# Kernel optimization log

Measured on AMD Instinct MI355X. Metric: run time of the kernel, lower is better.

The kernel has to match this reference:

```python
import jax, jax.numpy as jnp
import numpy as np

B, CITY, H, E, IN = 512, 100, 256, 256, 2
D2 = 2 * H  # num_directions * hidden_size
PEN = 1e6   # already_played_penalty


def _cell(x, h, c, Wih, Whh, b):
    # PyTorch LSTM cell, gate order i,f,g,o
    g = x @ Wih.T + h @ Whh.T + b
    i, f, gg, o = jnp.split(g, 4, axis=-1)
    c = jax.nn.sigmoid(f) * c + jax.nn.sigmoid(i) * jnp.tanh(gg)
    h = jax.nn.sigmoid(o) * jnp.tanh(c)
    return h, c


def _run_lstm(xs, Wih, Whh, b, reverse):
    # xs: [B, T, E] -> outputs [B, T, H], final (h, c)
    Bsz, hdim = xs.shape[0], Whh.shape[1]
    init = (jnp.zeros((Bsz, hdim), xs.dtype), jnp.zeros((Bsz, hdim), xs.dtype))
    def step(carry, x):
        h, c = _cell(x, carry[0], carry[1], Wih, Whh, b)
        return (h, c), h
    (h, c), hs = jax.lax.scan(step, init, jnp.swapaxes(xs, 0, 1), reverse=reverse)
    return jnp.swapaxes(hs, 0, 1), h, c


def setup_inputs() -> dict:
    key = jax.random.key(0)
    ks = iter(jax.random.split(key, 32))
    nrm = lambda shape: 0.1 * jax.random.normal(next(ks), shape, dtype=jnp.float32)
    return {
        "inputs": jax.random.normal(next(ks), (B, CITY, IN), dtype=jnp.float32),
        "test_roads": jax.random.randint(next(ks), (B, CITY), 0, CITY, dtype=jnp.int32),
        "W_embed": nrm((E, IN)),
        "enc_Wih_f": nrm((4 * H, E)), "enc_Whh_f": nrm((4 * H, H)), "enc_b_f": nrm((4 * H,)),
        "enc_Wih_b": nrm((4 * H, E)), "enc_Whh_b": nrm((4 * H, H)), "enc_b_b": nrm((4 * H,)),
        "dec_Wih_f": nrm((4 * H, D2)), "dec_Whh_f": nrm((4 * H, H)), "dec_b_f": nrm((4 * H,)),
        "dec_Wih_b": nrm((4 * H, D2)), "dec_Whh_b": nrm((4 * H, H)), "dec_b_b": nrm((4 * H,)),
        "W_ref": nrm((D2, D2)), "W_q": nrm((D2, D2)), "v": nrm((D2,)),
        "W_ref2": nrm((D2, D2)), "W_q2": nrm((D2, D2)), "v2": nrm((D2,)),
    }


def _forward(inputs, test_roads, W_embed,
             enc_Wih_f, enc_Whh_f, enc_b_f, enc_Wih_b, enc_Whh_b, enc_b_b,
             dec_Wih_f, dec_Whh_f, dec_b_f, dec_Wih_b, dec_Whh_b, dec_b_b,
             W_ref, W_q, v, W_ref2, W_q2, v2):
    Bsz, city, _ = inputs.shape
    emb = inputs @ W_embed.T                                  # [B, city, E]
    enc_f, hf0, cf0 = _run_lstm(emb, enc_Wih_f, enc_Whh_f, enc_b_f, False)
    enc_b, hb0, cb0 = _run_lstm(emb, enc_Wih_b, enc_Whh_b, enc_b_b, True)
    Enc = jnp.concatenate([enc_f, enc_b], axis=-1)            # [B, city, D2]
    # dropout p=0 -> Enc is loop-invariant; hoist the two ref projections
    ref1 = Enc @ W_ref.T                                      # [B, city, D2]
    ref2 = Enc @ W_ref2.T                                     # [B, city, D2]

    def step(carry, tgt):
        x, hf, cf, hb, cb, played, loss = carry
        hf, cf = _cell(x, hf, cf, dec_Wih_f, dec_Whh_f, dec_b_f)
        hb, cb = _cell(x, hb, cb, dec_Wih_b, dec_Whh_b, dec_b_b)
        dec_out = jnp.concatenate([hf, hb], axis=-1)          # [B, D2]
        ow = jnp.tanh(ref1 + (dec_out @ W_q.T)[:, None, :]) @ v - PEN * played   # [B, city]
        aw = jax.nn.softmax(jnp.tanh(ref2 + (x @ W_q2.T)[:, None, :]) @ v2, axis=1)
        sel = jnp.argmax(ow, axis=1)                          # [B]
        x_new = jnp.einsum('bj,bjk->bk', aw, Enc)             # [B, D2]
        played = played + jax.nn.one_hot(sel, city, dtype=played.dtype)
        ce = jax.nn.logsumexp(ow, axis=1) - jnp.take_along_axis(ow, tgt[:, None], axis=1)[:, 0]
        return (x_new, hf, cf, hb, cb, played, loss + ce), None

    x0 = jnp.zeros((Bsz, Enc.shape[-1]), inputs.dtype)
    played0 = jnp.zeros((Bsz, city), inputs.dtype)
    loss0 = jnp.zeros((Bsz,), inputs.dtype)
    carry, _ = jax.lax.scan(step, (x0, hf0, cf0, hb0, cb0, played0, loss0),
                            test_roads.T.astype(jnp.int32))
    return carry[-1]                                          # path_loss [B]


def reference(inputs, test_roads, W_embed,
              enc_Wih_f, enc_Whh_f, enc_b_f, enc_Wih_b, enc_Whh_b, enc_b_b,
              dec_Wih_f, dec_Whh_f, dec_b_f, dec_Wih_b, dec_Whh_b, dec_b_b,
              W_ref, W_q, v, W_ref2, W_q2, v2):
    return _forward(inputs, test_roads, W_embed,
                    enc_Wih_f, enc_Whh_f, enc_b_f, enc_Wih_b, enc_Whh_b, enc_b_b,
                    dec_Wih_f, dec_Whh_f, dec_b_f, dec_Wih_b, dec_Whh_b, dec_b_b,
                    W_ref, W_q, v, W_ref2, W_q2, v2)
```

## Files before the change

kernel.cpp:

```cpp
#include <hip/hip_runtime.h>
#include <hip/hip_fp16.h>
#include <math.h>

namespace {
constexpr int Bn  = 512;
constexpr int Tn  = 100;
constexpr int Hn  = 256;
constexpr int En  = 256;
constexpr int D2n = 512;
constexpr int G4n = 1024;
constexpr float PENf = 1e6f;
constexpr size_t BIGN = (size_t)Bn * Tn * D2n;
constexpr int FLAG_STRIDE = 32;
constexpr int DBLK = 896;
constexpr size_t BAR_UINTS = (256 + DBLK) * FLAG_STRIDE + 64;
}

using short8  = __attribute__((ext_vector_type(8))) short;
using us8     = __attribute__((ext_vector_type(8))) unsigned short;
using floatx4 = __attribute__((ext_vector_type(4))) float;

template<typename T> __device__ __forceinline__ float cvt_to_f(T x);
template<> __device__ __forceinline__ float cvt_to_f<float>(float x) { return x; }
template<> __device__ __forceinline__ float cvt_to_f<__half>(__half x) {
  return __half2float(x);
}
template<typename T> __device__ __forceinline__ T cvt_from_f(float x);
template<> __device__ __forceinline__ float cvt_from_f<float>(float x) { return x; }
template<> __device__ __forceinline__ __half cvt_from_f<__half>(float x) {
  return __float2half(x);
}
__device__ __forceinline__ float h2f_bits(unsigned short b) {
  __half_raw r; r.x = b; return __half2float(__half(r));
}
__device__ __forceinline__ float fast_exp(float x) {
  return __builtin_amdgcn_exp2f(x * 1.44269504088896340736f);
}
__device__ __forceinline__ float sigmoidf(float x) {
  return __builtin_amdgcn_rcpf(1.0f + fast_exp(-x));
}
__device__ __forceinline__ float fast_tanhf(float x) {
  return 1.0f - 2.0f * __builtin_amdgcn_rcpf(fast_exp(2.0f * x) + 1.0f);
}

__device__ __forceinline__ float loadf_dev(const float* p) {
  return __uint_as_float(__hip_atomic_load((const unsigned*)p, __ATOMIC_RELAXED,
                                           __HIP_MEMORY_SCOPE_AGENT));
}
__device__ __forceinline__ void storef_dev(float* p, float v) {
  __hip_atomic_store((unsigned*)p, __float_as_uint(v), __ATOMIC_RELAXED,
                     __HIP_MEMORY_SCOPE_AGENT);
}
__device__ __forceinline__ float4 load4_dev(const float* p) {
  const unsigned long long a = __hip_atomic_load((const unsigned long long*)p,
      __ATOMIC_RELAXED, __HIP_MEMORY_SCOPE_AGENT);
  const unsigned long long b = __hip_atomic_load((const unsigned long long*)p + 1,
      __ATOMIC_RELAXED, __HIP_MEMORY_SCOPE_AGENT);
  float4 r;
  r.x = __uint_as_float((unsigned)a);  r.y = __uint_as_float((unsigned)(a >> 32));
  r.z = __uint_as_float((unsigned)b);  r.w = __uint_as_float((unsigned)(b >> 32));
  return r;
}
__device__ __forceinline__ void store2_dev(float* p, const float2 v) {
  const unsigned long long a = (unsigned long long)__float_as_uint(v.x) |
                               ((unsigned long long)__float_as_uint(v.y) << 32);
  __hip_atomic_store((unsigned long long*)p, a, __ATOMIC_RELAXED,
                     __HIP_MEMORY_SCOPE_AGENT);
}
template<typename CT> __device__ __forceinline__ CT load_dev(const CT* p);
template<> __device__ __forceinline__ float load_dev<float>(const float* p) {
  return loadf_dev(p);
}
template<> __device__ __forceinline__ __half load_dev<__half>(const __half* p) {
  unsigned short u = __hip_atomic_load((const unsigned short*)p, __ATOMIC_RELAXED,
                                       __HIP_MEMORY_SCOPE_AGENT);
  __half_raw r; r.x = u; return (__half)r;
}
template<typename CT> __device__ __forceinline__ void store_dev(CT* p, CT v);
template<> __device__ __forceinline__ void store_dev<float>(float* p, float v) {
  storef_dev(p, v);
}
template<> __device__ __forceinline__ void store_dev<__half>(__half* p, __half v) {
  __half_raw r = *reinterpret_cast<__half_raw*>(&v);
  __hip_atomic_store((unsigned short*)p, r.x, __ATOMIC_RELAXED,
                     __HIP_MEMORY_SCOPE_AGENT);
}

__device__ __forceinline__ void split2(float x, short& h, short& l) {
  const unsigned u  = __float_as_uint(x);
  const unsigned hu = u & 0xffff0000u;
  h = (short)(hu >> 16);
  const float r = x - __uint_as_float(hu);
  l = (short)((__float_as_uint(r) + 0x8000u) >> 16);
}
__device__ __forceinline__ void store4split(const float4 v, short* hp, short* lp) {
  short h0, h1, h2, h3, l0, l1, l2, l3;
  split2(v.x, h0, l0); split2(v.y, h1, l1);
  split2(v.z, h2, l2); split2(v.w, h3, l3);
  *(short4*)hp = make_short4(h0, h1, h2, h3);
  *(short4*)lp = make_short4(l0, l1, l2, l3);
}

__device__ __forceinline__ void grid_sync256(unsigned* flags, unsigned* release,
                                             unsigned no) {
  __builtin_amdgcn_s_waitcnt(0);
  __syncthreads();
  if (blockIdx.x == 0) {
    const int tid = threadIdx.x;
    if (tid > 0) {
      while (__hip_atomic_load(&flags[tid * FLAG_STRIDE], __ATOMIC_RELAXED,
                               __HIP_MEMORY_SCOPE_AGENT) < no)
        __builtin_amdgcn_s_sleep(1);
    }
    __syncthreads();
    if (tid == 0)
      __hip_atomic_store(release, no, __ATOMIC_RELAXED, __HIP_MEMORY_SCOPE_AGENT);
  } else {
    if (threadIdx.x == 0) {
      __hip_atomic_store(&flags[blockIdx.x * FLAG_STRIDE], no, __ATOMIC_RELAXED,
                         __HIP_MEMORY_SCOPE_AGENT);
      while (__hip_atomic_load(release, __ATOMIC_RELAXED,
                               __HIP_MEMORY_SCOPE_AGENT) < no)
        __builtin_amdgcn_s_sleep(2);
    }
    __syncthreads();
  }
}

__device__ __forceinline__ void grid_syncD(unsigned* flags, unsigned* release,
                                           unsigned no) {
  __builtin_amdgcn_s_waitcnt(0);
  __syncthreads();
  if (blockIdx.x == 0) {
    for (int i = threadIdx.x; i < DBLK; i += 256) {
      if (i > 0) {
        while (__hip_atomic_load(&flags[i * FLAG_STRIDE], __ATOMIC_RELAXED,
                                 __HIP_MEMORY_SCOPE_AGENT) < no)
          __builtin_amdgcn_s_sleep(1);
      }
    }
    __syncthreads();
    if (threadIdx.x == 0)
      __hip_atomic_store(release, no, __ATOMIC_RELAXED, __HIP_MEMORY_SCOPE_AGENT);
  } else {
    if (threadIdx.x == 0) {
      __hip_atomic_store(&flags[blockIdx.x * FLAG_STRIDE], no, __ATOMIC_RELAXED,
                         __HIP_MEMORY_SCOPE_AGENT);
      while (__hip_atomic_load(release, __ATOMIC_RELAXED,
                               __HIP_MEMORY_SCOPE_AGENT) < no)
        __builtin_amdgcn_s_sleep(2);
    }
    __syncthreads();
  }
}

template<typename CT, bool ACC, int NT, bool CSC>
__device__ __forceinline__ void gemm64v2(short* smem,
    const float* A, int lda, int m0,
    const float* B, int ldb, int n0, int K,
    CT* Cbase, size_t crstride, int tid) {
  constexpr int BPL  = NT * 128;
  constexpr int BSZ  = NT * 512;
  constexpr int BUFS = 4096 + 2 * BSZ;
  const int lane = tid & 63, wave = tid >> 6, qm = lane & 15, quad = lane >> 4;
  const int ra = tid >> 3, c4 = tid & 7, j0 = (c4 & 1) * 4, gq = c4 >> 1;
  const int a0 = gq * 512 + ra * 8 + j0;
  const int a1 = gq * 512 + (ra + 32) * 8 + j0;
  const int b0 = gq * BPL + ra * 8 + j0;
  const int b1 = gq * BPL + (ra + 32) * 8 + j0;
  const int CN = K >> 5;

  floatx4 acc[NT];
#pragma unroll
  for (int nt = 0; nt < NT; ++nt) acc[nt] = (floatx4){0.f, 0.f, 0.f, 0.f};

  float4 Aa0, Aa1, Ba0, Ba1, Ab0, Ab1, Bb0, Bb1;
  auto ld = [&](int c, float4& x0, float4& x1, float4& y0, float4& y1) {
    const int k0 = c * 32 + c4 * 4;
    x0 = load4_dev(A + (size_t)(m0 + ra) * lda + k0);
    x1 = load4_dev(A + (size_t)(m0 + ra + 32) * lda + k0);
    y0 = *(const float4*)(B + (size_t)(n0 + ra) * ldb + k0);
    if (NT == 4)
      y1 = *(const float4*)(B + (size_t)(n0 + ra + 32) * ldb + k0);
  };
  auto st = [&](short* bp, const float4& x0, const float4& x1,
                const float4& y0, const float4& y1) {
    store4split(x0, bp + a0, bp + 2048 + a0);
    store4split(x1, bp + a1, bp + 2048 + a1);
    store4split(y0, bp + 4096 + b0, bp + 4096 + BSZ + b0);
    if (NT == 4) store4split(y1, bp + 4096 + b1, bp + 4096 + BSZ + b1);
  };
  auto mm = [&](const short* bp) {
    const int abase = quad * 512 + (wave * 16 + qm) * 8;
    const short8 ah = *(const short8*)&bp[abase];
    const short8 al = *(const short8*)&bp[2048 + abase];
#pragma unroll
    for (int nt = 0; nt < NT; ++nt) {
      const int bb = quad * BPL + (nt * 16 + qm) * 8;
      const short8 bh = *(const short8*)&bp[4096 + bb];
      const short8 bl = *(const short8*)&bp[4096 + BSZ + bb];
      acc[nt] = __builtin_amdgcn_mfma_f32_16x16x32_bf16(ah, bh, acc[nt], 0, 0, 0);
      acc[nt] = __builtin_amdgcn_mfma_f32_16x16x32_bf16(ah, bl, acc[nt], 0, 0, 0);
      acc[nt] = __builtin_amdgcn_mfma_f32_16x16x32_bf16(al, bh, acc[nt], 0, 0, 0);
    }
  };

  ld(0, Aa0, Aa1, Ba0, Ba1);
  if (CN > 1) ld(1, Ab0, Ab1, Bb0, Bb1);
  st(smem, Aa0, Aa1, Ba0, Ba1);
  __syncthreads();
  for (int c = 0; c < CN; c += 2) {
    if (c + 2 < CN) ld(c + 2, Aa0, Aa1, Ba0, Ba1);
    mm(smem);
    if (c + 1 < CN) st(smem + BUFS, Ab0, Ab1, Bb0, Bb1);
    __syncthreads();
    if (c + 1 < CN) {
      if (c + 3 < CN) ld(c + 3, Ab0, Ab1, Bb0, Bb1);
      mm(smem + BUFS);
      if (c + 2 < CN) st(smem, Aa0, Aa1, Ba0, Ba1);
      __syncthreads();
    }
  }

#pragma unroll
  for (int nt = 0; nt < NT; ++nt)
#pragma unroll
    for (int r2 = 0; r2 < 4; ++r2) {
      const int m = wave * 16 + quad * 4 + r2, n = nt * 16 + qm;
      CT* cp = Cbase + (size_t)m * crstride + n;
      float o = acc[nt][r2];
      if (CSC) {
        if (ACC) o += cvt_to_f<CT>(load_dev<CT>(cp));
        store_dev<CT>(cp, cvt_from_f<CT>(o));
      } else {
        if (ACC) o += cvt_to_f<CT>(*cp);
        *cp = cvt_from_f<CT>(o);
      }
    }
}

__device__ __forceinline__ void gates_gemm_v2(floatx4 acc[4], short* smem,
    const float* A1, int lda1, const float* B1, int ldb1, int K1,
    const float* A2, int lda2, const float* B2, int ldb2, int K2,
    int m0, int hoff, int tid) {
  const int lane = tid & 63, wave = tid >> 6, qm = lane & 15, quad = lane >> 4;
  const int ra = tid >> 3, c4 = tid & 7, j0 = (c4 & 1) * 4, gq = c4 >> 1;
  const int a0 = gq * 512 + ra * 8 + j0;
  const int a1 = gq * 512 + (ra + 32) * 8 + j0;
  const int g0 = (ra >> 4) * Hn + hoff + (ra & 15);
  const int g1 = ((ra + 32) >> 4) * Hn + hoff + ((ra + 32) & 15);
  const int C1 = K1 >> 5;
  const int C2 = A2 ? (K2 >> 5) : 0;
  const int CN = C1 + C2;

  float4 Aa0, Aa1, Ba0, Ba1, Ab0, Ab1, Bb0, Bb1;
  auto ld = [&](int c, float4& x0, float4& x1, float4& y0, float4& y1) {
    const float* A; const float* B; int lda, ldb, k0;
    if (c < C1) { A = A1; B = B1; lda = lda1; ldb = ldb1; k0 = c * 32; }
    else        { A = A2; B = B2; lda = lda2; ldb = ldb2; k0 = (c - C1) * 32; }
    k0 += c4 * 4;
    x0 = load4_dev(A + (size_t)(m0 + ra) * lda + k0);
    x1 = load4_dev(A + (size_t)(m0 + ra + 32) * lda + k0);
    y0 = *(const float4*)(B + (size_t)g0 * ldb + k0);
    y1 = *(const float4*)(B + (size_t)g1 * ldb + k0);
  };
  auto st2 = [&](short* bp, const float4& x0, const float4& x1,
                 const float4& y0, const float4& y1) {
    store4split(x0, bp + a0, bp + 2048 + a0);
    store4split(x1, bp + a1, bp + 2048 + a1);
    store4split(y0, bp + 4096 + a0, bp + 6144 + a0);
    store4split(y1, bp + 4096 + a1, bp + 6144 + a1);
  };
  auto mm = [&](const short* bp) {
    const int abase = quad * 512 + (wave * 16 + qm) * 8;
    const short8 ah = *(const short8*)&bp[abase];
    const short8 al = *(const short8*)&bp[2048 + abase];
#pragma unroll
    for (int gg = 0; gg < 4; ++gg) {
      const int bb = quad * 512 + (gg * 16 + qm) * 8;
      const short8 bh = *(const short8*)&bp[4096 + bb];
      const short8 bl = *(const short8*)&bp[6144 + bb];
      acc[gg] = __builtin_amdgcn_mfma_f32_16x16x32_bf16(ah, bh, acc[gg], 0, 0, 0);
      acc[gg] = __builtin_amdgcn_mfma_f32_16x16x32_bf16(ah, bl, acc[gg], 0, 0, 0);
      acc[gg] = __builtin_amdgcn_mfma_f32_16x16x32_bf16(al, bh, acc[gg], 0, 0, 0);
    }
  };

  if (CN <= 0) return;
  ld(0, Aa0, Aa1, Ba0, Ba1);
  if (CN > 1) ld(1, Ab0, Ab1, Bb0, Bb1);
  st2(smem, Aa0, Aa1, Ba0, Ba1);
  __syncthreads();
  for (int c = 0; c < CN; c += 2) {
    if (c + 2 < CN) ld(c + 2, Aa0, Aa1, Ba0, Ba1);
    mm(smem);
    if (c + 1 < CN) st2(smem + 8192, Ab0, Ab1, Bb0, Bb1);
    __syncthreads();
    if (c + 1 < CN) {
      if (c + 3 < CN) ld(c + 3, Ab0, Ab1, Bb0, Bb1);
      mm(smem + 8192);
      if (c + 2 < CN) st2(smem, Aa0, Aa1, Ba0, Ba1);
      __syncthreads();
    }
  }
}

__global__ void weff_kernel(const float* Wih_f, const float* Wih_b,
                            const float* W_embed, float* weff_f, float* weff_b) {
  const int gidx = blockIdx.x * 256 + threadIdx.x;
  if (gidx >= G4n) return;
  float f0 = 0.f, f1 = 0.f, b0 = 0.f, b1 = 0.f;
  for (int e = 0; e < En; ++e) {
    const float w0 = W_embed[e * 2 + 0];
    const float w1 = W_embed[e * 2 + 1];
    const float wf = Wih_f[gidx * En + e];
    const float wb = Wih_b[gidx * En + e];
    f0 = fmaf(wf, w0, f0); f1 = fmaf(wf, w1, f1);
    b0 = fmaf(wb, w0, b0); b1 = fmaf(wb, w1, b1);
  }
  weff_f[gidx * 2 + 0] = f0; weff_f[gidx * 2 + 1] = f1;
  weff_b[gidx * 2 + 0] = b0; weff_b[gidx * 2 + 1] = b1;
}

template<typename ET, typename RT1, typename RT2>
struct EncP {
  const float* inputs;
  const float* Whh_f; const float* Whh_b;
  const float* b_f; const float* b_b;
  const float* weff_f; const float* weff_b;
  const float* W_ref; const float* W_ref2;
  float* hbuf;
  float* c_dec;
  float* dec_out0;
  ET* Enc; RT1* ref1; RT2* ref2;
  unsigned* flags; unsigned* release;
};

template<typename ET, typename RT1, typename RT2>
__global__ __launch_bounds__(256, 1) void enc_coop(EncP<ET, RT1, RT2> P) {
  __shared__ __align__(16) short smem[16384];
  const int bid = blockIdx.x, tid = threadIdx.x;
  const int dir = bid >> 7, btile = (bid >> 4) & 7, hs = bid & 15;
  const int r_ref = (bid >> 7) & 1, r_dir = (bid >> 6) & 1;
  const int r_bt = (bid >> 3) & 7, r_ns = bid & 7;
  const int lane = tid & 63, wave = tid >> 6, qm = lane & 15, quad = lane >> 4;
  const int hcol = hs * 16 + qm;
  const float* Whh  = dir ? P.Whh_b : P.Whh_f;
  const float* bias = dir ? P.b_b : P.b_f;
  const float* weff = dir ? P.weff_b : P.weff_f;
  float c_reg[4] = {0.f, 0.f, 0.f, 0.f};
  float h_reg[4] = {0.f, 0.f, 0.f, 0.f};
  unsigned sync_no = 0;

  auto ref_job = [&](const float* hpar, int pos) {
    const float* hsrc = hpar + (size_t)r_dir * (Bn * Hn);
    if (r_ref == 0)
      gemm64v2<RT1, true, 4, true>(smem, hsrc, Hn, r_bt * 64,
                             P.W_ref + r_dir * Hn, D2n, r_ns * 64, Hn,
                             P.ref1 + (size_t)(r_bt * 64) * Tn * D2n + (size_t)pos * D2n + r_ns * 64,
                             (size_t)Tn * D2n, tid);
    else
      gemm64v2<RT2, true, 4, true>(smem, hsrc, Hn, r_bt * 64,
                             P.W_ref2 + r_dir * Hn, D2n, r_ns * 64, Hn,
                             P.ref2 + (size_t)(r_bt * 64) * Tn * D2n + (size_t)pos * D2n + r_ns * 64,
                             (size_t)Tn * D2n, tid);
  };

  for (int t = 0; t < Tn; ++t) {
    const float* hprev = P.hbuf + (size_t)((t - 1) & 1) * (2 * Bn * Hn);
    if (t > 0) ref_job(hprev, r_dir ? (Tn - t) : (t - 1));
    floatx4 acc[4];
#pragma unroll
    for (int gg = 0; gg < 4; ++gg) acc[gg] = (floatx4){0.f, 0.f, 0.f, 0.f};
    if (t > 0)
      gates_gemm_v2(acc, smem, hprev + (size_t)dir * (Bn * Hn), Hn, Whh, Hn, Hn,
                    nullptr, 0, nullptr, 0, 0, btile * 64, hs * 16, tid);
    const int tcur = dir ? (Tn - 1 - t) : t;
    float xa[4], xb2[4];
#pragma unroll
    for (int r2 = 0; r2 < 4; ++r2) {
      const int m = btile * 64 + wave * 16 + quad * 4 + r2;
      xa[r2]  = P.inputs[(size_t)m * (Tn * 2) + tcur * 2 + 0];
      xb2[r2] = P.inputs[(size_t)m * (Tn * 2) + tcur * 2 + 1];
    }
    float gv[4][4];
#pragma unroll
    for (int gg = 0; gg < 4; ++gg) {
      const int grow = gg * Hn + hcol;
      const float bn = bias[grow];
      const float w20 = weff[grow * 2], w21 = weff[grow * 2 + 1];
#pragma unroll
      for (int r2 = 0; r2 < 4; ++r2) {
        float o = acc[gg][r2] + bn;
        o = fmaf(xa[r2], w20, fmaf(xb2[r2], w21, o));
        gv[gg][r2] = o;
      }
    }
    float* hdst = P.hbuf + (size_t)(t & 1) * (2 * Bn * Hn) + (size_t)dir * (Bn * Hn);
    const int tt = dir ? (Tn - 1 - t) : t;
#pragma unroll
    for (int r2 = 0; r2 < 4; ++r2) {
      const float cn = sigmoidf(gv[1][r2]) * c_reg[r2] +
                       sigmoidf(gv[0][r2]) * fast_tanhf(gv[2][r2]);
      c_reg[r2] = cn;
      const float hn = sigmoidf(gv[3][r2]) * fast_tanhf(cn);
      h_reg[r2] = hn;
      const int m = btile * 64 + wave * 16 + quad * 4 + r2;
      storef_dev(&hdst[(size_t)m * Hn + hcol], hn);
      store_dev<ET>(&P.Enc[(size_t)m * Tn * D2n + (size_t)tt * D2n + dir * Hn + hcol],
                    cvt_from_f<ET>(hn));
    }
    grid_sync256(P.flags, P.release, ++sync_no);
  }
  ref_job(P.hbuf + (size_t)1 * (2 * Bn * Hn), r_dir ? 0 : (Tn - 1));
#pragma unroll
  for (int r2 = 0; r2 < 4; ++r2) {
    const int m = btile * 64 + wave * 16 + quad * 4 + r2;
    P.dec_out0[(size_t)m * D2n + dir * Hn + hcol] = h_reg[r2];
    P.c_dec[((size_t)dir * Bn + m) * Hn + hcol] = c_reg[r2];
  }
}

template<typename ET, typename RT1, typename RT2>
struct DecP {
  const int* test_roads;
  const float* Wih_f; const float* Whh_f; const float* b_f;
  const float* Wih_b; const float* Whh_b; const float* b_b;
  const float* W_q; const float* W_q2; const float* v; const float* v2;
  const ET* Enc; const RT1* ref1; const RT2* ref2;
  float* dec_out;
  float* xb;
  float* qb; float* q2b;
  const float* c_init;
  float* loss;
  unsigned* flags; unsigned* release;
};

template<typename ET, typename RT1, typename RT2>
__global__ __launch_bounds__(256, 4) void dec_coop(DecP<ET, RT1, RT2> P) {
  __shared__ __align__(16) short smem[16384];
  __shared__ float sl[104], playedl[104];
  __shared__ float wmax[4], wsum[4], dpart[4];
  __shared__ int   widx[4];
  __shared__ float lossl;
  const int bid = blockIdx.x, tid = threadIdx.x;
  const int lane = tid & 63, wave = tid >> 6, qm = lane & 15, quad = lane >> 4;
  const int role = (bid < 256) ? 0 : (bid < 384 ? 1 : 2);

  const int dir = (bid >> 7) & 1, btile = (bid >> 4) & 7, hs = bid & 15;
  const int hcol = hs * 16 + qm;
  const float* Wih  = dir ? P.Wih_b : P.Wih_f;
  const float* Whh  = dir ? P.Whh_b : P.Whh_f;
  const float* bias = dir ? P.b_b : P.b_f;
  float c_reg[4] = {0.f, 0.f, 0.f, 0.f};
  if (role == 0) {
#pragma unroll
    for (int r2 = 0; r2 < 4; ++r2) {
      const int m = btile * 64 + wave * 16 + quad * 4 + r2;
      c_reg[r2] = P.c_init[((size_t)dir * Bn + m) * Hn + hcol];
    }
  }
  const int gidx = bid - 256, pbt = gidx >> 4, pn = gidx & 15;
  const int b = bid - 384;
  if (role == 2) {
    if (tid < Tn) playedl[tid] = 0.f;
    if (tid == 0) lossl = 0.f;
  }
  unsigned sync_no = 0;
  __syncthreads();

  auto s1_fused = [&](int u) {
    const int e = lane * 8;
    const float4 qa = load4_dev(P.qb + (size_t)b * D2n + e);
    const float4 qc = load4_dev(P.qb + (size_t)b * D2n + e + 4);
    const float4 va = *(const float4*)(P.v + e);
    const float4 vb2 = *(const float4*)(P.v + e + 4);
    const float q[8]  = {qa.x, qa.y, qa.z, qa.w, qc.x, qc.y, qc.z, qc.w};
    const float vv[8] = {va.x, va.y, va.z, va.w, vb2.x, vb2.y, vb2.z, vb2.w};
    const unsigned short* pr = (const unsigned short*)P.ref1 +
        (size_t)b * Tn * D2n + (size_t)(wave * 25) * D2n + e;
    us8 r0 = *(const us8*)pr;
    us8 r1 = *(const us8*)(pr + (size_t)D2n);
    us8 r2v = *(const us8*)(pr + (size_t)2 * D2n);
    float bmax = -INFINITY, sume = 0.f; int bidx = 0;
    for (int jj = 0; jj < 25; ++jj) {
      const int row = wave * 25 + jj;
      float a = 0.f;
#pragma unroll
      for (int k = 0; k < 8; ++k)
        a = fmaf(vv[k], fast_tanhf(h2f_bits(r0[k]) + q[k]), a);
      r0 = r1; r1 = r2v;
      if (jj + 3 < 25) r2v = *(const us8*)(pr + (size_t)(jj + 3) * D2n);
#pragma unroll
      for (int off = 32; off > 0; off >>= 1) a += __shfl_xor(a, off, 64);
      if (lane == 0) sl[row] = a;
      const float ow = a - PENf * playedl[row];
      if (ow > bmax) { bmax = ow; bidx = row; }
      sume += fast_exp(ow - 16.f);
    }
    if (lane == 0) { wmax[wave] = bmax; widx[wave] = bidx; wsum[wave] = sume; }
    __syncthreads();
    if (tid == 0) {
      float bv = wmax[0], es = wsum[0]; int bi = widx[0];
#pragma unroll
      for (int w = 1; w < 4; ++w) {
        es += wsum[w];
        if (wmax[w] > bv) { bv = wmax[w]; bi = widx[w]; }
      }
      const int tgt = P.test_roads[b * Tn + u];
      const float owt = sl[tgt] - PENf * playedl[tgt];
      lossl += (16.f + __logf(es)) - owt;
      playedl[bi] += 1.f;
    }
  };

  auto s2x_fused = [&]() {
    const int e = lane * 8;
    const float4 qa = load4_dev(P.q2b + (size_t)b * D2n + e);
    const float4 qc = load4_dev(P.q2b + (size_t)b * D2n + e + 4);
    const float4 va = *(const float4*)(P.v2 + e);
    const float4 vb2 = *(const float4*)(P.v2 + e + 4);
    const float q[8]  = {qa.x, qa.y, qa.z, qa.w, qc.x, qc.y, qc.z, qc.w};
    const float vv[8] = {va.x, va.y, va.z, va.w, vb2.x, vb2.y, vb2.z, vb2.w};
    const unsigned short* pr = (const unsigned short*)P.ref2 +
        (size_t)b * Tn * D2n + (size_t)(wave * 25) * D2n + e;
    const unsigned short* pe = (const unsigned short*)P.Enc +
        (size_t)b * Tn * D2n + (size_t)(wave * 25) * D2n + e;
    us8 r0 = *(const us8*)pr;
    us8 r1 = *(const us8*)(pr + (size_t)D2n);
    us8 r2v = *(const us8*)(pr + (size_t)2 * D2n);
    us8 e0 = *(const us8*)pe;
    us8 e1 = *(const us8*)(pe + (size_t)D2n);
    us8 e2v = *(const us8*)(pe + (size_t)2 * D2n);
    float xacc[8];
#pragma unroll
    for (int k = 0; k < 8; ++k) xacc[k] = 0.f;
    float den = 0.f;
    for (int jj = 0; jj < 25; ++jj) {
      float a = 0.f;
#pragma unroll
      for (int k = 0; k < 8; ++k)
        a = fmaf(vv[k], fast_tanhf(h2f_bits(r0[k]) + q[k]), a);
      r0 = r1; r1 = r2v;
      if (jj + 3 < 25) r2v = *(const us8*)(pr + (size_t)(jj + 3) * D2n);
#pragma unroll
      for (int off = 32; off > 0; off >>= 1) a += __shfl_xor(a, off, 64);
      const float w = fast_exp(a - 16.f);
      den += w;
#pragma unroll
      for (int k = 0; k < 8; ++k)
        xacc[k] = fmaf(w, h2f_bits(e0[k]), xacc[k]);
      e0 = e1; e1 = e2v;
      if (jj + 3 < 25) e2v = *(const us8*)(pe + (size_t)(jj + 3) * D2n);
    }
    float* xpart = (float*)smem;
#pragma unroll
    for (int k = 0; k < 8; ++k) xpart[wave * 512 + e + k] = xacc[k];
    if (lane == 0) dpart[wave] = den;
    __syncthreads();
    {
      const float dsum = dpart[0] + dpart[1] + dpart[2] + dpart[3];
      const float inv = __builtin_amdgcn_rcpf(dsum);
      const int c = tid * 2;
      float2 s;
      s.x = (xpart[c] + xpart[512 + c] + xpart[1024 + c] + xpart[1536 + c]) * inv;
      s.y = (xpart[c + 1] + xpart[512 + c + 1] + xpart[1024 + c + 1] +
             xpart[1536 + c + 1]) * inv;
      store2_dev(&P.xb[(size_t)b * D2n + c], s);
    }
  };

  for (int t = 0; t < Tn; ++t) {
    const float* dcur = P.dec_out + (size_t)(t & 1) * (Bn * D2n);
    float* dnext = P.dec_out + (size_t)((t + 1) & 1) * (Bn * D2n);
    if (role == 0) {
      floatx4 acc[4];
#pragma unroll
      for (int gg = 0; gg < 4; ++gg) acc[gg] = (floatx4){0.f, 0.f, 0.f, 0.f};
      gates_gemm_v2(acc, smem, P.xb, D2n, Wih, D2n, D2n,
                    dcur + dir * Hn, D2n, Whh, Hn, Hn, btile * 64, hs * 16, tid);
#pragma unroll
      for (int gg = 0; gg < 4; ++gg) {
        const float bn = bias[gg * Hn + hcol];
#pragma unroll
        for (int r2 = 0; r2 < 4; ++r2) acc[gg][r2] += bn;
      }
#pragma unroll
      for (int r2 = 0; r2 < 4; ++r2) {
        const float cn = sigmoidf(acc[1][r2]) * c_reg[r2] +
                         sigmoidf(acc[0][r2]) * fast_tanhf(acc[2][r2]);
        c_reg[r2] = cn;
        const float hn = sigmoidf(acc[3][r2]) * fast_tanhf(cn);
        const int m = btile * 64 + wave * 16 + quad * 4 + r2;
        storef_dev(&dnext[(size_t)m * D2n + dir * Hn + hcol], hn);
      }
    } else if (role == 1) {
      gemm64v2<float, false, 2, true>(smem, P.xb, D2n, pbt * 64,
                                      P.W_q2, D2n, pn * 32, D2n,
                                      P.q2b + (size_t)(pbt * 64) * D2n + pn * 32,
                                      D2n, tid);
    } else if (t > 0) {
      s1_fused(t - 1);
    }
    grid_syncD(P.flags, P.release, ++sync_no);
    if (role == 1) {
      gemm64v2<float, false, 2, true>(smem, dnext, D2n, pbt * 64,
                                      P.W_q, D2n, pn * 32, D2n,
                                      P.qb + (size_t)(pbt * 64) * D2n + pn * 32,
                                      D2n, tid);
    } else if (role == 2) {
      s2x_fused();
    }
    grid_syncD(P.flags, P.release, ++sync_no);
  }
  if (role == 2) {
    s1_fused(Tn - 1);
    if (tid == 0) P.loss[b] = lossl;
  }
}

static void run_all(void* const* d_in, void* d_out, char* ws, hipStream_t stream) {
  using ET = __half; using RT1 = __half; using RT2 = __half;
  const float* inputs     = (const float*)d_in[0];
  const int*   test_roads = (const int*)d_in[1];
  const float* W_embed    = (const float*)d_in[2];
  const float* enc_Wih_f  = (const float*)d_in[3];
  const float* enc_Whh_f  = (const float*)d_in[4];
  const float* enc_b_f    = (const float*)d_in[5];
  const float* enc_Wih_b  = (const float*)d_in[6];
  const float* enc_Whh_b  = (const float*)d_in[7];
  const float* enc_b_b    = (const float*)d_in[8];
  const float* dec_Wih_f  = (const float*)d_in[9];
  const float* dec_Whh_f  = (const float*)d_in[10];
  const float* dec_b_f    = (const float*)d_in[11];
  const float* dec_Wih_b  = (const float*)d_in[12];
  const float* dec_Whh_b  = (const float*)d_in[13];
  const float* dec_b_b    = (const float*)d_in[14];
  const float* W_ref      = (const float*)d_in[15];
  const float* W_q        = (const float*)d_in[16];
  const float* v          = (const float*)d_in[17];
  const float* W_ref2     = (const float*)d_in[18];
  const float* W_q2       = (const float*)d_in[19];
  const float* v2         = (const float*)d_in[20];

  char* p0 = ws;
  ET*  Enc  = (ET*)p0;  p0 += BIGN * sizeof(ET);
  RT1* ref1 = (RT1*)p0; p0 += BIGN * sizeof(RT1);
  RT2* ref2 = (RT2*)p0; p0 += BIGN * sizeof(RT2);
  unsigned* flagsE = (unsigned*)p0;
  unsigned* relE   = flagsE + 256 * FLAG_STRIDE;
  unsigned* flagsD = relE + 32;
  unsigned* relD   = flagsD + DBLK * FLAG_STRIDE;
  float* xb      = (float*)(p0 + BAR_UINTS * 4);
  float* dec_out = xb + Bn * D2n;
  float* hbuf    = dec_out + 2 * Bn * D2n;
  float* c_dec   = hbuf + 4 * Bn * Hn;
  float* qb      = c_dec + 2 * Bn * Hn;
  float* q2b     = qb + Bn * D2n;
  float* weff_f  = q2b + Bn * D2n;
  float* weff_b  = weff_f + G4n * 2;

  hipMemsetAsync(ref1, 0, BIGN * (sizeof(RT1) + sizeof(RT2)), stream);
  hipMemsetAsync(flagsE, 0, BAR_UINTS * 4 + (size_t)Bn * D2n * 4, stream);

  weff_kernel<<<G4n / 256, 256, 0, stream>>>(enc_Wih_f, enc_Wih_b, W_embed,
                                             weff_f, weff_b);

  EncP<ET, RT1, RT2> ep = { inputs, enc_Whh_f, enc_Whh_b, enc_b_f, enc_b_b,
                            weff_f, weff_b, W_ref, W_ref2,
                            hbuf, c_dec, dec_out, Enc, ref1, ref2,
                            flagsE, relE };
  enc_coop<ET, RT1, RT2><<<256, 256, 0, stream>>>(ep);

  DecP<ET, RT1, RT2> dp = { test_roads,
                            dec_Wih_f, dec_Whh_f, dec_b_f,
                            dec_Wih_b, dec_Whh_b, dec_b_b,
                            W_q, W_q2, v, v2,
                            Enc, ref1, ref2,
                            dec_out, xb, qb, q2b, c_dec,
                            (float*)d_out, flagsD, relD };
  dec_coop<ET, RT1, RT2><<<DBLK, 256, 0, stream>>>(dp);
}

extern "C" void kernel_launch(void* const* d_in, const int* in_sizes, int n_in,
                              void* d_out, int out_size, void* d_ws, size_t ws_size,
                              hipStream_t stream) {
  (void)in_sizes; (void)n_in; (void)out_size; (void)ws_size;
  run_all(d_in, d_out, (char*)d_ws, stream);
}
```

Before: 7.862 ms.

## Split encoder grid into separate recurrence and ref-projection block groups

The encoder cooperative kernel grows from 256 to 512 blocks. The first 256 blocks run only the LSTM recurrence, and the other 256 compute the W_ref/W_ref2 projections of the previous step's hidden state. Before, each block did both jobs one after the other inside the critical recurrence step; now the projection work runs alongside the recurrence. The cost is a grid barrier over twice as many blocks and a need for two blocks per CU (launch bounds raised to 2), which may pressure registers and LDS.

```diff
diff --git a/kernel.cpp b/kernel.cpp
--- a/kernel.cpp
+++ b/kernel.cpp
@@ -12,8 +12,9 @@
 constexpr float PENf = 1e6f;
 constexpr size_t BIGN = (size_t)Bn * Tn * D2n;
 constexpr int FLAG_STRIDE = 32;
+constexpr int EBLK = 512;
 constexpr int DBLK = 896;
-constexpr size_t BAR_UINTS = (256 + DBLK) * FLAG_STRIDE + 64;
+constexpr size_t BAR_UINTS = (EBLK + DBLK) * FLAG_STRIDE + 64;
 }
 
 using short8  = __attribute__((ext_vector_type(8))) short;
@@ -101,38 +102,13 @@
   *(short4*)lp = make_short4(l0, l1, l2, l3);
 }
 
-__device__ __forceinline__ void grid_sync256(unsigned* flags, unsigned* release,
-                                             unsigned no) {
-  __builtin_amdgcn_s_waitcnt(0);
-  __syncthreads();
-  if (blockIdx.x == 0) {
-    const int tid = threadIdx.x;
-    if (tid > 0) {
-      while (__hip_atomic_load(&flags[tid * FLAG_STRIDE], __ATOMIC_RELAXED,
-                               __HIP_MEMORY_SCOPE_AGENT) < no)
-        __builtin_amdgcn_s_sleep(1);
-    }
-    __syncthreads();
-    if (tid == 0)
-      __hip_atomic_store(release, no, __ATOMIC_RELAXED, __HIP_MEMORY_SCOPE_AGENT);
-  } else {
-    if (threadIdx.x == 0) {
-      __hip_atomic_store(&flags[blockIdx.x * FLAG_STRIDE], no, __ATOMIC_RELAXED,
-                         __HIP_MEMORY_SCOPE_AGENT);
-      while (__hip_atomic_load(release, __ATOMIC_RELAXED,
-                               __HIP_MEMORY_SCOPE_AGENT) < no)
-        __builtin_amdgcn_s_sleep(2);
-    }
-    __syncthreads();
-  }
-}
-
-__device__ __forceinline__ void grid_syncD(unsigned* flags, unsigned* release,
+template<int NB>
+__device__ __forceinline__ void grid_syncN(unsigned* flags, unsigned* release,
                                            unsigned no) {
   __builtin_amdgcn_s_waitcnt(0);
   __syncthreads();
   if (blockIdx.x == 0) {
-    for (int i = threadIdx.x; i < DBLK; i += 256) {
+    for (int i = threadIdx.x; i < NB; i += 256) {
       if (i > 0) {
         while (__hip_atomic_load(&flags[i * FLAG_STRIDE], __ATOMIC_RELAXED,
                                  __HIP_MEMORY_SCOPE_AGENT) < no)
@@ -337,12 +313,14 @@
 };
 
 template<typename ET, typename RT1, typename RT2>
-__global__ __launch_bounds__(256, 1) void enc_coop(EncP<ET, RT1, RT2> P) {
+__global__ __launch_bounds__(256, 2) void enc_coop(EncP<ET, RT1, RT2> P) {
   __shared__ __align__(16) short smem[16384];
   const int bid = blockIdx.x, tid = threadIdx.x;
-  const int dir = bid >> 7, btile = (bid >> 4) & 7, hs = bid & 15;
-  const int r_ref = (bid >> 7) & 1, r_dir = (bid >> 6) & 1;
-  const int r_bt = (bid >> 3) & 7, r_ns = bid & 7;
+  const bool gr = bid < 256;
+  const int dir = (bid >> 7) & 1, btile = (bid >> 4) & 7, hs = bid & 15;
+  const int rbid = bid - 256;
+  const int r_ref = (rbid >> 7) & 1, r_dir = (rbid >> 6) & 1;
+  const int r_bt = (rbid >> 3) & 7, r_ns = rbid & 7;
   const int lane = tid & 63, wave = tid >> 6, qm = lane & 15, quad = lane >> 4;
   const int hcol = hs * 16 + qm;
   const float* Whh  = dir ? P.Whh_b : P.Whh_f;
@@ -368,56 +346,62 @@
 
   for (int t = 0; t < Tn; ++t) {
     const float* hprev = P.hbuf + (size_t)((t - 1) & 1) * (2 * Bn * Hn);
-    if (t > 0) ref_job(hprev, r_dir ? (Tn - t) : (t - 1));
-    floatx4 acc[4];
-#pragma unroll
-    for (int gg = 0; gg < 4; ++gg) acc[gg] = (floatx4){0.f, 0.f, 0.f, 0.f};
-    if (t > 0)
-      gates_gemm_v2(acc, smem, hprev + (size_t)dir * (Bn * Hn), Hn, Whh, Hn, Hn,
-                    nullptr, 0, nullptr, 0, 0, btile * 64, hs * 16, tid);
-    const int tcur = dir ? (Tn - 1 - t) : t;
-    float xa[4], xb2[4];
+    if (gr) {
+      floatx4 acc[4];
+#pragma unroll
+      for (int gg = 0; gg < 4; ++gg) acc[gg] = (floatx4){0.f, 0.f, 0.f, 0.f};
+      if (t > 0)
+        gates_gemm_v2(acc, smem, hprev + (size_t)dir * (Bn * Hn), Hn, Whh, Hn, Hn,
+                      nullptr, 0, nullptr, 0, 0, btile * 64, hs * 16, tid);
+      const int tcur = dir ? (Tn - 1 - t) : t;
+      float xa[4], xb2[4];
+#pragma unroll
+      for (int r2 = 0; r2 < 4; ++r2) {
+        const int m = btile * 64 + wave * 16 + quad * 4 + r2;
+        xa[r2]  = P.inputs[(size_t)m * (Tn * 2) + tcur * 2 + 0];
+        xb2[r2] = P.inputs[(size_t)m * (Tn * 2) + tcur * 2 + 1];
+      }
+      float gv[4][4];
+#pragma unroll
+      for (int gg = 0; gg < 4; ++gg) {
+        const int grow = gg * Hn + hcol;
+        const float bn = bias[grow];
+        const float w20 = weff[grow * 2], w21 = weff[grow * 2 + 1];
+#pragma unroll
+        for (int r2 = 0; r2 < 4; ++r2) {
+          float o = acc[gg][r2] + bn;
+          o = fmaf(xa[r2], w20, fmaf(xb2[r2], w21, o));
+          gv[gg][r2] = o;
+        }
+      }
+      float* hdst = P.hbuf + (size_t)(t & 1) * (2 * Bn * Hn) + (size_t)dir * (Bn * Hn);
+      const int tt = dir ? (Tn - 1 - t) : t;
+#pragma unroll
+      for (int r2 = 0; r2 < 4; ++r2) {
+        const float cn = sigmoidf(gv[1][r2]) * c_reg[r2] +
+                         sigmoidf(gv[0][r2]) * fast_tanhf(gv[2][r2]);
+        c_reg[r2] = cn;
+        const float hn = sigmoidf(gv[3][r2]) * fast_tanhf(cn);
+        h_reg[r2] = hn;
+        const int m = btile * 64 + wave * 16 + quad * 4 + r2;
+        storef_dev(&hdst[(size_t)m * Hn + hcol], hn);
+        store_dev<ET>(&P.Enc[(size_t)m * Tn * D2n + (size_t)tt * D2n + dir * Hn + hcol],
+                      cvt_from_f<ET>(hn));
+      }
+    } else if (t > 0) {
+      ref_job(hprev, r_dir ? (Tn - t) : (t - 1));
+    }
+    grid_syncN<EBLK>(P.flags, P.release, ++sync_no);
+  }
+  if (!gr) {
+    ref_job(P.hbuf + (size_t)1 * (2 * Bn * Hn), r_dir ? 0 : (Tn - 1));
+  } else {
 #pragma unroll
     for (int r2 = 0; r2 < 4; ++r2) {
       const int m = btile * 64 + wave * 16 + quad * 4 + r2;
-      xa[r2]  = P.inputs[(size_t)m * (Tn * 2) + tcur * 2 + 0];
-      xb2[r2] = P.inputs[(size_t)m * (Tn * 2) + tcur * 2 + 1];
-    }
-    float gv[4][4];
-#pragma unroll
-    for (int gg = 0; gg < 4; ++gg) {
-      const int grow = gg * Hn + hcol;
-      const float bn = bias[grow];
-      const float w20 = weff[grow * 2], w21 = weff[grow * 2 + 1];
-#pragma unroll
-      for (int r2 = 0; r2 < 4; ++r2) {
-        float o = acc[gg][r2] + bn;
-        o = fmaf(xa[r2], w20, fmaf(xb2[r2], w21, o));
-        gv[gg][r2] = o;
-      }
-    }
-    float* hdst = P.hbuf + (size_t)(t & 1) * (2 * Bn * Hn) + (size_t)dir * (Bn * Hn);
-    const int tt = dir ? (Tn - 1 - t) : t;
-#pragma unroll
-    for (int r2 = 0; r2 < 4; ++r2) {
-      const float cn = sigmoidf(gv[1][r2]) * c_reg[r2] +
-                       sigmoidf(gv[0][r2]) * fast_tanhf(gv[2][r2]);
-      c_reg[r2] = cn;
-      const float hn = sigmoidf(gv[3][r2]) * fast_tanhf(cn);
-      h_reg[r2] = hn;
-      const int m = btile * 64 + wave * 16 + quad * 4 + r2;
-      storef_dev(&hdst[(size_t)m * Hn + hcol], hn);
-      store_dev<ET>(&P.Enc[(size_t)m * Tn * D2n + (size_t)tt * D2n + dir * Hn + hcol],
-                    cvt_from_f<ET>(hn));
-    }
-    grid_sync256(P.flags, P.release, ++sync_no);
-  }
-  ref_job(P.hbuf + (size_t)1 * (2 * Bn * Hn), r_dir ? 0 : (Tn - 1));
-#pragma unroll
-  for (int r2 = 0; r2 < 4; ++r2) {
-    const int m = btile * 64 + wave * 16 + quad * 4 + r2;
-    P.dec_out0[(size_t)m * D2n + dir * Hn + hcol] = h_reg[r2];
-    P.c_dec[((size_t)dir * Bn + m) * Hn + hcol] = c_reg[r2];
+      P.dec_out0[(size_t)m * D2n + dir * Hn + hcol] = h_reg[r2];
+      P.c_dec[((size_t)dir * Bn + m) * Hn + hcol] = c_reg[r2];
+    }
   }
 }
 
@@ -602,7 +586,7 @@
     } else if (t > 0) {
       s1_fused(t - 1);
     }
-    grid_syncD(P.flags, P.release, ++sync_no);
+    grid_syncN<DBLK>(P.flags, P.release, ++sync_no);
     if (role == 1) {
       gemm64v2<float, false, 2, true>(smem, dnext, D2n, pbt * 64,
                                       P.W_q, D2n, pn * 32, D2n,
@@ -611,7 +595,7 @@
     } else if (role == 2) {
       s2x_fused();
     }
-    grid_syncD(P.flags, P.release, ++sync_no);
+    grid_syncN<DBLK>(P.flags, P.release, ++sync_no);
   }
   if (role == 2) {
     s1_fused(Tn - 1);
@@ -648,7 +632,7 @@
   RT1* ref1 = (RT1*)p0; p0 += BIGN * sizeof(RT1);
   RT2* ref2 = (RT2*)p0; p0 += BIGN * sizeof(RT2);
   unsigned* flagsE = (unsigned*)p0;
-  unsigned* relE   = flagsE + 256 * FLAG_STRIDE;
+  unsigned* relE   = flagsE + EBLK * FLAG_STRIDE;
   unsigned* flagsD = relE + 32;
   unsigned* relD   = flagsD + DBLK * FLAG_STRIDE;
   float* xb      = (float*)(p0 + BAR_UINTS * 4);
@@ -670,7 +654,7 @@
                             weff_f, weff_b, W_ref, W_ref2,
                             hbuf, c_dec, dec_out, Enc, ref1, ref2,
                             flagsE, relE };
-  enc_coop<ET, RT1, RT2><<<256, 256, 0, stream>>>(ep);
+  enc_coop<ET, RT1, RT2><<<EBLK, 256, 0, stream>>>(ep);
 
   DecP<ET, RT1, RT2> dp = { test_roads,
                             dec_Wih_f, dec_Whh_f, dec_b_f,
```

Measured after the change: 7.418 ms. -5.6%, faster.
